# Optimization experiments

Hardware: AMD Instinct MI355X
Metric: run time of the kernel (lower is better)

The kernel has to match this reference:

```python
import jax, jax.numpy as jnp
import numpy as np

K = 3          # spatial kernel partitions
EPS = 1e-5     # BatchNorm eps


def setup_inputs() -> dict:
    key = jax.random.key(0)
    ks = jax.random.split(key, 5)
    N, C_in, T, V = 32, 64, 512, 27
    C_out = 128
    return {
        "x": jax.random.normal(ks[0], (N, C_in, T, V), dtype=jnp.float32),
        "len_x": 512,
        "conv_w": jax.random.normal(ks[1], (C_out * K, C_in, 1, 1), dtype=jnp.float32) * 0.05,
        "conv_b": jax.random.normal(ks[2], (C_out * K,), dtype=jnp.float32) * 0.05,
        "A": jax.random.uniform(ks[3], (K, V, V), dtype=jnp.float32),
        "gamma": jnp.ones((C_out,), dtype=jnp.float32),
        "beta": jnp.zeros((C_out,), dtype=jnp.float32),
    }


def reference(x, len_x, conv_w, conv_b, A, gamma, beta):
    # Pointwise conv (kernel (1,1)): [N,C_in,T,V] x [K*C_out,C_in] -> [N,K*C_out,T,V]
    w = conv_w[:, :, 0, 0]
    y = jnp.einsum('nctv,oc->notv', x, w) + conv_b[None, :, None, None]
    n, kc, t, v = y.shape
    y = y.reshape(n, K, kc // K, t, v)
    # Graph aggregation over adjacency partitions
    z = jnp.einsum('nkctv,kvw->nctw', y, A)
    # BatchNorm2d (training mode: batch stats, biased variance) + ReLU
    mean = jnp.mean(z, axis=(0, 2, 3), keepdims=True)
    var = jnp.mean((z - mean) ** 2, axis=(0, 2, 3), keepdims=True)
    zn = (z - mean) * jax.lax.rsqrt(var + EPS)
    out = zn * gamma[None, :, None, None] + beta[None, :, None, None]
    return jax.nn.relu(out)
```

## Files before the change

kernel.cpp:

```cpp
#include <hip/hip_runtime.h>
#include <cstdint>
#include <cstddef>

#define NT_TOTAL 16384
#define R_NT 8
#define NBLK 2048
#define CNT_F 442368.0f

#define XA_OFF 0
#define XA_STRIDE 400
#define R2_OFF 102400
#define XS_STRIDE 80
#define WBT_STRIDE 400
#define CB_OFF 153600
#define SA_OFF 155136
#define ST_OFF 155520
#define LDS_BYTES 156544
#define ZL_STRIDE 260

typedef __attribute__((ext_vector_type(8))) short short8;
typedef __attribute__((ext_vector_type(4))) float f32x4;

__device__ __forceinline__ unsigned short f2bf(float f) {
  unsigned int u = __float_as_uint(f);
  u = u + 0x7FFFu + ((u >> 16) & 1u);
  return (unsigned short)(u >> 16);
}
__device__ __forceinline__ float bf2f(unsigned short b) {
  return __uint_as_float(((unsigned int)b) << 16);
}

template <bool ZBF16>
__global__ __launch_bounds__(512, 2) void gcn_k1(
    const float* __restrict__ x, const float* __restrict__ cw,
    const float* __restrict__ cb, const float* __restrict__ A,
    float* __restrict__ zout_f32, unsigned short* __restrict__ zout_bf16,
    float* __restrict__ partial) {
  extern __shared__ char smem[];
  const int tid = threadIdx.x;
  const int lane = tid & 63;
  const int wid = tid >> 6;
  const int blk = blockIdx.x;
  const int nt0 = blk * R_NT;

  const int ci = tid & 63;
  const int r = wid;
  const int ntI = nt0 + r;
  const int nI = ntI >> 9;
  const int tI = ntI & 511;
  const float* xr = x + ((size_t)(nI * 64 + ci) * 512 + tI) * 27;
  float xrow[27];
#pragma unroll
  for (int v = 0; v < 27; ++v) xrow[v] = xr[v];

  float2 wreg[24];
  {
    const float2* cw2 = (const float2*)cw;
#pragma unroll
    for (int i = 0; i < 24; ++i) {
      const int p = i * 512 + tid;
      const int c = p / 96;
      const int kp = p % 96;
      const int k = kp >> 5;
      const int cip = kp & 31;
      wreg[i] = cw2[(k * 128 + c) * 32 + cip];
    }
  }

  short8 aop[3][2];
#pragma unroll
  for (int k = 0; k < 3; ++k)
#pragma unroll
    for (int mt = 0; mt < 2; ++mt) {
      const int wr = mt * 16 + (lane & 15);
#pragma unroll
      for (int j = 0; j < 8; ++j) {
        const int v = (lane >> 4) * 8 + j;
        float val = (wr < 27 && v < 27) ? A[k * 729 + v * 27 + wr] : 0.f;
        aop[k][mt][j] = (short)f2bf(val);
      }
    }

  if (tid < 256) ((float*)(smem + ST_OFF))[tid] = 0.f;
  if (tid < 384) ((float*)(smem + CB_OFF))[tid] = cb[tid];
  if (tid < 81) {
    const int k = tid / 27, w = tid % 27;
    float s = 0.f;
#pragma unroll
    for (int v = 0; v < 27; ++v) s += A[k * 729 + v * 27 + w];
    ((float*)(smem + SA_OFF))[k * 32 + w] = s;
  }
  {
    char* base = smem + R2_OFF + r * (64 * XS_STRIDE) + ci * XS_STRIDE;
#pragma unroll
    for (int i = 0; i < 16; ++i) {
      const int v0 = 2 * i, v1 = 2 * i + 1;
      unsigned int b0 = (v0 < 27) ? (unsigned int)f2bf(xrow[v0]) : 0u;
      unsigned int b1 = (v1 < 27) ? (unsigned int)f2bf(xrow[v1]) : 0u;
      *(unsigned int*)(base + i * 4) = b0 | (b1 << 16);
    }
  }
  __syncthreads();

  {
    const int r2 = wid;
    short8 bfr[4];
#pragma unroll
    for (int nt2 = 0; nt2 < 4; ++nt2) {
      const int ci2 = nt2 * 16 + (lane & 15);
      bfr[nt2] = *(const short8*)(smem + R2_OFF + r2 * (64 * XS_STRIDE) +
                                  ci2 * XS_STRIDE + (lane >> 4) * 16);
    }
#pragma unroll
    for (int k = 0; k < 3; ++k)
#pragma unroll
      for (int mt = 0; mt < 2; ++mt)
#pragma unroll
        for (int nt2 = 0; nt2 < 4; ++nt2) {
          f32x4 d = {0.f, 0.f, 0.f, 0.f};
          d = __builtin_amdgcn_mfma_f32_16x16x32_bf16(aop[k][mt], bfr[nt2], d, 0, 0, 0);
          const int ciW = nt2 * 16 + (lane & 15);
#pragma unroll
          for (int reg = 0; reg < 4; ++reg) {
            const int w = mt * 16 + (lane >> 4) * 4 + reg;
            if (w < 27) {
              const int m = r2 * 32 + w;
              *(unsigned short*)(smem + XA_OFF + m * XA_STRIDE + (k * 64 + ciW) * 2) =
                  f2bf(d[reg]);
            }
          }
        }
  }
  __syncthreads();

#pragma unroll
  for (int i = 0; i < 24; ++i) {
    const int p = i * 512 + tid;
    const int c = p / 96;
    const int kp = p % 96;
    unsigned int b0 = f2bf(wreg[i].x);
    unsigned int b1 = f2bf(wreg[i].y);
    *(unsigned int*)(smem + R2_OFF + c * WBT_STRIDE + kp * 4) = b0 | (b1 << 16);
  }
  __syncthreads();

  const int mgrp = wid >> 1;
  const int ngrp = wid & 1;
  f32x4 acc[4][4];
#pragma unroll
  for (int a = 0; a < 4; ++a)
#pragma unroll
    for (int b = 0; b < 4; ++b) acc[a][b] = (f32x4){0.f, 0.f, 0.f, 0.f};

#pragma unroll
  for (int ks = 0; ks < 6; ++ks) {
    short8 afr[4], bfr2[4];
#pragma unroll
    for (int mt = 0; mt < 4; ++mt) {
      const int m = mgrp * 64 + mt * 16 + (lane & 15);
      afr[mt] = *(const short8*)(smem + XA_OFF + m * XA_STRIDE + ks * 64 + (lane >> 4) * 16);
    }
#pragma unroll
    for (int ntt = 0; ntt < 4; ++ntt) {
      const int c = ngrp * 64 + ntt * 16 + (lane & 15);
      bfr2[ntt] = *(const short8*)(smem + R2_OFF + c * WBT_STRIDE + ks * 64 + (lane >> 4) * 16);
    }
#pragma unroll
    for (int mt = 0; mt < 4; ++mt)
#pragma unroll
      for (int ntt = 0; ntt < 4; ++ntt)
        acc[mt][ntt] =
            __builtin_amdgcn_mfma_f32_16x16x32_bf16(afr[mt], bfr2[ntt], acc[mt][ntt], 0, 0, 0);
  }
  __syncthreads();

  {
    const float* cbl = (const float*)(smem + CB_OFF);
    const float* sal = (const float*)(smem + SA_OFF);
    float* stats = (float*)(smem + ST_OFF);
    float cb0[4], cb1[4], cb2[4];
    int cc[4];
#pragma unroll
    for (int ntt = 0; ntt < 4; ++ntt) {
      cc[ntt] = ngrp * 64 + ntt * 16 + (lane & 15);
      cb0[ntt] = cbl[cc[ntt]];
      cb1[ntt] = cbl[128 + cc[ntt]];
      cb2[ntt] = cbl[256 + cc[ntt]];
    }
    float s1[4] = {0.f, 0.f, 0.f, 0.f}, s2[4] = {0.f, 0.f, 0.f, 0.f};
#pragma unroll
    for (int mt = 0; mt < 4; ++mt)
#pragma unroll
      for (int reg = 0; reg < 4; ++reg) {
        const int m = mgrp * 64 + mt * 16 + (lane >> 4) * 4 + reg;
        const int w = m & 31;
        if (w < 27) {
          const float sa0 = sal[w], sa1 = sal[32 + w], sa2 = sal[64 + w];
#pragma unroll
          for (int ntt = 0; ntt < 4; ++ntt) {
            float val = acc[mt][ntt][reg] + cb0[ntt] * sa0 + cb1[ntt] * sa1 + cb2[ntt] * sa2;
            s1[ntt] += val;
            s2[ntt] += val * val;
            *(unsigned short*)(smem + m * ZL_STRIDE + cc[ntt] * 2) = f2bf(val);
          }
        }
      }
#pragma unroll
    for (int ntt = 0; ntt < 4; ++ntt) {
      float a1 = s1[ntt], a2 = s2[ntt];
      a1 += __shfl_xor(a1, 16); a1 += __shfl_xor(a1, 32);
      a2 += __shfl_xor(a2, 16); a2 += __shfl_xor(a2, 32);
      if ((lane & 48) == 0) {
        atomicAdd(&stats[cc[ntt]], a1);
        atomicAdd(&stats[128 + cc[ntt]], a2);
      }
    }
  }
  __syncthreads();

  {
    const int n3 = nt0 >> 9;
    const int t0 = nt0 & 511;
    if (ZBF16) {
#pragma unroll 4
      for (int i = 0; i < 27; ++i) {
        const int idx = i * 512 + tid;
        const int c = idx / 108;
        const int jp = idx % 108;
        const int j0 = jp * 2, j1 = j0 + 1;
        const int tl0 = j0 / 27, w0 = j0 % 27;
        const int tl1 = j1 / 27, w1 = j1 % 27;
        unsigned int b0 = *(unsigned short*)(smem + (tl0 * 32 + w0) * ZL_STRIDE + c * 2);
        unsigned int b1 = *(unsigned short*)(smem + (tl1 * 32 + w1) * ZL_STRIDE + c * 2);
        const size_t base_e = ((size_t)(n3 * 128 + c) * 512 + t0) * 27;
        *(unsigned int*)((char*)zout_bf16 + base_e * 2 + (size_t)jp * 4) = b0 | (b1 << 16);
      }
    } else {
#pragma unroll 4
      for (int i = 0; i < 54; ++i) {
        const int idx = i * 512 + tid;
        const int c = idx / 216;
        const int j = idx % 216;
        const int tl = j / 27, w = j % 27;
        float v = bf2f(*(unsigned short*)(smem + (tl * 32 + w) * ZL_STRIDE + c * 2));
        zout_f32[((size_t)(n3 * 128 + c) * 512 + (t0 + tl)) * 27 + w] = v;
      }
    }
    if (tid < 256) partial[blk * 256 + tid] = ((float*)(smem + ST_OFF))[tid];
  }
}

__global__ __launch_bounds__(256) void gcn_k2(const float* __restrict__ partial,
                                              const float* __restrict__ gamma,
                                              const float* __restrict__ beta,
                                              float* __restrict__ ss) {
  __shared__ float lds[256];
  const int tid = threadIdx.x;
  float a0 = 0.f, a1 = 0.f, a2 = 0.f, a3 = 0.f;
  for (int b = 0; b < NBLK; b += 4) {
    a0 += partial[(b + 0) * 256 + tid];
    a1 += partial[(b + 1) * 256 + tid];
    a2 += partial[(b + 2) * 256 + tid];
    a3 += partial[(b + 3) * 256 + tid];
  }
  lds[tid] = (a0 + a1) + (a2 + a3);
  __syncthreads();
  if (tid < 128) {
    const float inv = 1.f / CNT_F;
    float mean = lds[tid] * inv;
    float var = lds[128 + tid] * inv - mean * mean;
    float rstd = rsqrtf(var + 1e-5f);
    float sc = gamma[tid] * rstd;
    ss[tid] = sc;
    ss[128 + tid] = beta[tid] - mean * sc;
  }
}

template <bool ZBF16>
__global__ __launch_bounds__(256) void gcn_k3(const unsigned short* __restrict__ zbf,
                                              float* __restrict__ out,
                                              const float* __restrict__ ss) {
  const int blk = blockIdx.x;
  const int tid = threadIdx.x;
  const int c = blk & 127;
  const float sc = ss[c];
  const float sh = ss[128 + c];
  float4* op = (float4*)out + (size_t)blk * 3456;
  if (ZBF16) {
    const ushort4* zp = (const ushort4*)zbf + (size_t)blk * 3456;
#pragma unroll 4
    for (int i = 0; i < 14; ++i) {
      const int idx = i * 256 + tid;
      if (idx < 3456) {
        ushort4 zv = zp[idx];
        float4 o;
        o.x = fmaxf(bf2f(zv.x) * sc + sh, 0.f);
        o.y = fmaxf(bf2f(zv.y) * sc + sh, 0.f);
        o.z = fmaxf(bf2f(zv.z) * sc + sh, 0.f);
        o.w = fmaxf(bf2f(zv.w) * sc + sh, 0.f);
        op[idx] = o;
      }
    }
  } else {
#pragma unroll 4
    for (int i = 0; i < 14; ++i) {
      const int idx = i * 256 + tid;
      if (idx < 3456) {
        float4 zv = op[idx];
        float4 o;
        o.x = fmaxf(zv.x * sc + sh, 0.f);
        o.y = fmaxf(zv.y * sc + sh, 0.f);
        o.z = fmaxf(zv.z * sc + sh, 0.f);
        o.w = fmaxf(zv.w * sc + sh, 0.f);
        op[idx] = o;
      }
    }
  }
}

extern "C" void kernel_launch(void* const* d_in, const int* in_sizes, int n_in,
                              void* d_out, int out_size, void* d_ws, size_t ws_size,
                              hipStream_t stream) {
  (void)in_sizes; (void)n_in; (void)out_size;
  const float* x = (const float*)d_in[0];
  const float* cw = (const float*)d_in[2];
  const float* cb = (const float*)d_in[3];
  const float* A = (const float*)d_in[4];
  const float* gm = (const float*)d_in[5];
  const float* bt = (const float*)d_in[6];
  float* out = (float*)d_out;

  const size_t Z_BYTES = (size_t)56623104 * 2;
  const size_t PART_F = (size_t)NBLK * 256;
  const bool zbf16 = ws_size >= Z_BYTES + PART_F * 4 + 1024;

  if (zbf16) {
    unsigned short* zws = (unsigned short*)d_ws;
    float* partial = (float*)((char*)d_ws + Z_BYTES);
    float* ss = partial + PART_F;
    hipFuncSetAttribute((const void*)gcn_k1<true>,
                        hipFuncAttributeMaxDynamicSharedMemorySize, LDS_BYTES);
    gcn_k1<true><<<NBLK, 512, LDS_BYTES, stream>>>(x, cw, cb, A, nullptr, zws, partial);
    gcn_k2<<<1, 256, 0, stream>>>(partial, gm, bt, ss);
    gcn_k3<true><<<4096, 256, 0, stream>>>(zws, out, ss);
  } else {
    float* partial = (float*)d_ws;
    float* ss = partial + PART_F;
    hipFuncSetAttribute((const void*)gcn_k1<false>,
                        hipFuncAttributeMaxDynamicSharedMemorySize, LDS_BYTES);
    gcn_k1<false><<<NBLK, 512, LDS_BYTES, stream>>>(x, cw, cb, A, out, nullptr, partial);
    gcn_k2<<<1, 256, 0, stream>>>(partial, gm, bt, ss);
    gcn_k3<false><<<4096, 256, 0, stream>>>(nullptr, out, ss);
  }
}
```

Before: 542.2 us.

## Precompute bf16 weights and bias, shrink tiles, raise occupancy, split stats reduction

```diff
diff --git a/kernel.cpp b/kernel.cpp
--- a/kernel.cpp
+++ b/kernel.cpp
@@ -2,21 +2,24 @@
 #include <cstdint>
 #include <cstddef>
 
-#define NT_TOTAL 16384
-#define R_NT 8
-#define NBLK 2048
+#define R_NT 4
+#define NBLK 4096
 #define CNT_F 442368.0f
 
-#define XA_OFF 0
 #define XA_STRIDE 400
-#define R2_OFF 102400
+#define XS_OFF 51200
 #define XS_STRIDE 80
-#define WBT_STRIDE 400
-#define CB_OFF 153600
-#define SA_OFF 155136
-#define ST_OFF 155520
-#define LDS_BYTES 156544
-#define ZL_STRIDE 260
+#define ST_OFF 71680
+#define LDS_BYTES 72704
+#define ZL_STRIDE 264
+
+#define Z_BYTES   113246208ull
+#define WBT_SZ    49152
+#define B2_SZ     16384
+#define AOP_SZ    6144
+#define SS_SZ     1024
+#define PART2_SZ  65536
+#define PART_SZ   4194304
 
 typedef __attribute__((ext_vector_type(8))) short short8;
 typedef __attribute__((ext_vector_type(4))) float f32x4;
@@ -30,10 +33,49 @@
   return __uint_as_float(((unsigned int)b) << 16);
 }
 
+__global__ __launch_bounds__(256) void gcn_k0(const float* __restrict__ cw,
+                                              const float* __restrict__ cb,
+                                              const float* __restrict__ A,
+                                              unsigned short* __restrict__ wbt,
+                                              float* __restrict__ bias2,
+                                              unsigned short* __restrict__ aopt) {
+  const int idx = blockIdx.x * 256 + threadIdx.x;
+  if (idx < 12288) {
+    const int c = idx / 96, p = idx - c * 96;
+    const int k = p >> 5, ci0 = (p & 31) * 2;
+    const float* src = cw + ((size_t)(k * 128 + c)) * 64 + ci0;
+    ((unsigned int*)wbt)[idx] = (unsigned int)f2bf(src[0]) | ((unsigned int)f2bf(src[1]) << 16);
+  } else if (idx < 16384) {
+    const int e = idx - 12288;
+    const int c = e >> 5, w = e & 31;
+    float val = 0.f;
+    if (w < 27) {
+#pragma unroll
+      for (int k = 0; k < 3; ++k) {
+        float sa = 0.f;
+#pragma unroll
+        for (int v = 0; v < 27; ++v) sa += A[k * 729 + v * 27 + w];
+        val += cb[k * 128 + c] * sa;
+      }
+    }
+    bias2[e] = val;
+  } else if (idx < 17920) {
+    const int e2 = (idx - 16384) * 2;
+    const int k = e2 >> 10, rem = e2 & 1023;
+    const int mt = rem >> 9, rem2 = rem & 511;
+    const int ln = rem2 >> 3, j0 = rem2 & 7;
+    const int wr = mt * 16 + (ln & 15);
+    const int v0 = (ln >> 4) * 8 + j0, v1 = v0 + 1;
+    float f0 = (wr < 27 && v0 < 27) ? A[k * 729 + v0 * 27 + wr] : 0.f;
+    float f1 = (wr < 27 && v1 < 27) ? A[k * 729 + v1 * 27 + wr] : 0.f;
+    ((unsigned int*)aopt)[idx - 16384] = (unsigned int)f2bf(f0) | ((unsigned int)f2bf(f1) << 16);
+  }
+}
+
 template <bool ZBF16>
-__global__ __launch_bounds__(512, 2) void gcn_k1(
-    const float* __restrict__ x, const float* __restrict__ cw,
-    const float* __restrict__ cb, const float* __restrict__ A,
+__global__ __launch_bounds__(512, 4) void gcn_k1(
+    const float* __restrict__ x, const unsigned short* __restrict__ wbt,
+    const float* __restrict__ bias2, const unsigned short* __restrict__ aopt,
     float* __restrict__ zout_f32, unsigned short* __restrict__ zout_bf16,
     float* __restrict__ partial) {
   extern __shared__ char smem[];
@@ -42,169 +84,130 @@
   const int wid = tid >> 6;
   const int blk = blockIdx.x;
   const int nt0 = blk * R_NT;
-
-  const int ci = tid & 63;
-  const int r = wid;
-  const int ntI = nt0 + r;
-  const int nI = ntI >> 9;
-  const int tI = ntI & 511;
-  const float* xr = x + ((size_t)(nI * 64 + ci) * 512 + tI) * 27;
-  float xrow[27];
-#pragma unroll
-  for (int v = 0; v < 27; ++v) xrow[v] = xr[v];
-
-  float2 wreg[24];
+  const int n = nt0 >> 9;
+  const int t0 = nt0 & 511;
+
+  short8 aop[3][2];
+#pragma unroll
+  for (int k = 0; k < 3; ++k)
+#pragma unroll
+    for (int mt = 0; mt < 2; ++mt)
+      aop[k][mt] = *(const short8*)(aopt + ((k * 2 + mt) * 64 + lane) * 8);
+
   {
-    const float2* cw2 = (const float2*)cw;
-#pragma unroll
-    for (int i = 0; i < 24; ++i) {
-      const int p = i * 512 + tid;
-      const int c = p / 96;
-      const int kp = p % 96;
-      const int k = kp >> 5;
-      const int cip = kp & 31;
-      wreg[i] = cw2[(k * 128 + c) * 32 + cip];
-    }
-  }
-
-  short8 aop[3][2];
-#pragma unroll
-  for (int k = 0; k < 3; ++k)
-#pragma unroll
-    for (int mt = 0; mt < 2; ++mt) {
-      const int wr = mt * 16 + (lane & 15);
-#pragma unroll
-      for (int j = 0; j < 8; ++j) {
-        const int v = (lane >> 4) * 8 + j;
-        float val = (wr < 27 && v < 27) ? A[k * 729 + v * 27 + wr] : 0.f;
-        aop[k][mt][j] = (short)f2bf(val);
-      }
-    }
-
+    const int idx = tid >> 1, h = tid & 1;
+    const int r = idx >> 6, ci = idx & 63;
+    const float* xr = x + ((size_t)(n * 64 + ci) * 512 + t0 + r) * 27;
+    unsigned int* row = (unsigned int*)(smem + XS_OFF + (r * 64 + ci) * XS_STRIDE);
+    if (h == 0) {
+      float f[14];
+#pragma unroll
+      for (int v = 0; v < 14; ++v) f[v] = xr[v];
+#pragma unroll
+      for (int p = 0; p < 7; ++p)
+        row[p] = (unsigned int)f2bf(f[2 * p]) | ((unsigned int)f2bf(f[2 * p + 1]) << 16);
+    } else {
+      float f[13];
+#pragma unroll
+      for (int v = 0; v < 13; ++v) f[v] = xr[14 + v];
+#pragma unroll
+      for (int p = 7; p < 16; ++p) {
+        const int v0 = 2 * p - 14, v1 = v0 + 1;
+        unsigned int b0 = (v0 < 13) ? (unsigned int)f2bf(f[v0]) : 0u;
+        unsigned int b1 = (v1 < 13) ? (unsigned int)f2bf(f[v1]) : 0u;
+        row[p] = b0 | (b1 << 16);
+      }
+    }
+  }
   if (tid < 256) ((float*)(smem + ST_OFF))[tid] = 0.f;
-  if (tid < 384) ((float*)(smem + CB_OFF))[tid] = cb[tid];
-  if (tid < 81) {
-    const int k = tid / 27, w = tid % 27;
-    float s = 0.f;
-#pragma unroll
-    for (int v = 0; v < 27; ++v) s += A[k * 729 + v * 27 + w];
-    ((float*)(smem + SA_OFF))[k * 32 + w] = s;
-  }
+  __syncthreads();
+
   {
-    char* base = smem + R2_OFF + r * (64 * XS_STRIDE) + ci * XS_STRIDE;
-#pragma unroll
-    for (int i = 0; i < 16; ++i) {
-      const int v0 = 2 * i, v1 = 2 * i + 1;
-      unsigned int b0 = (v0 < 27) ? (unsigned int)f2bf(xrow[v0]) : 0u;
-      unsigned int b1 = (v1 < 27) ? (unsigned int)f2bf(xrow[v1]) : 0u;
-      *(unsigned int*)(base + i * 4) = b0 | (b1 << 16);
-    }
-  }
-  __syncthreads();
-
-  {
-    const int r2 = wid;
-    short8 bfr[4];
-#pragma unroll
-    for (int nt2 = 0; nt2 < 4; ++nt2) {
-      const int ci2 = nt2 * 16 + (lane & 15);
-      bfr[nt2] = *(const short8*)(smem + R2_OFF + r2 * (64 * XS_STRIDE) +
-                                  ci2 * XS_STRIDE + (lane >> 4) * 16);
+    const int r2 = wid >> 1, half = wid & 1;
+    short8 bfr[2];
+#pragma unroll
+    for (int nt2 = 0; nt2 < 2; ++nt2) {
+      const int ci2 = half * 32 + nt2 * 16 + (lane & 15);
+      bfr[nt2] = *(const short8*)(smem + XS_OFF + (r2 * 64 + ci2) * XS_STRIDE + (lane >> 4) * 16);
     }
 #pragma unroll
     for (int k = 0; k < 3; ++k)
 #pragma unroll
       for (int mt = 0; mt < 2; ++mt)
 #pragma unroll
-        for (int nt2 = 0; nt2 < 4; ++nt2) {
+        for (int nt2 = 0; nt2 < 2; ++nt2) {
           f32x4 d = {0.f, 0.f, 0.f, 0.f};
           d = __builtin_amdgcn_mfma_f32_16x16x32_bf16(aop[k][mt], bfr[nt2], d, 0, 0, 0);
-          const int ciW = nt2 * 16 + (lane & 15);
+          const int ciW = half * 32 + nt2 * 16 + (lane & 15);
+          const int wb = mt * 16 + (lane >> 4) * 4;
 #pragma unroll
           for (int reg = 0; reg < 4; ++reg) {
-            const int w = mt * 16 + (lane >> 4) * 4 + reg;
-            if (w < 27) {
-              const int m = r2 * 32 + w;
-              *(unsigned short*)(smem + XA_OFF + m * XA_STRIDE + (k * 64 + ciW) * 2) =
-                  f2bf(d[reg]);
-            }
+            const int m = r2 * 32 + wb + reg;
+            *(unsigned short*)(smem + m * XA_STRIDE + (k * 64 + ciW) * 2) = f2bf(d[reg]);
           }
         }
   }
   __syncthreads();
 
-#pragma unroll
-  for (int i = 0; i < 24; ++i) {
-    const int p = i * 512 + tid;
-    const int c = p / 96;
-    const int kp = p % 96;
-    unsigned int b0 = f2bf(wreg[i].x);
-    unsigned int b1 = f2bf(wreg[i].y);
-    *(unsigned int*)(smem + R2_OFF + c * WBT_STRIDE + kp * 4) = b0 | (b1 << 16);
-  }
-  __syncthreads();
-
   const int mgrp = wid >> 1;
   const int ngrp = wid & 1;
-  f32x4 acc[4][4];
-#pragma unroll
-  for (int a = 0; a < 4; ++a)
+  f32x4 acc[2][4];
+#pragma unroll
+  for (int a = 0; a < 2; ++a)
 #pragma unroll
     for (int b = 0; b < 4; ++b) acc[a][b] = (f32x4){0.f, 0.f, 0.f, 0.f};
 
-#pragma unroll
+#pragma unroll 2
   for (int ks = 0; ks < 6; ++ks) {
-    short8 afr[4], bfr2[4];
-#pragma unroll
-    for (int mt = 0; mt < 4; ++mt) {
-      const int m = mgrp * 64 + mt * 16 + (lane & 15);
-      afr[mt] = *(const short8*)(smem + XA_OFF + m * XA_STRIDE + ks * 64 + (lane >> 4) * 16);
+    short8 afr[2], bfrg[4];
+#pragma unroll
+    for (int mt = 0; mt < 2; ++mt) {
+      const int m = mgrp * 32 + mt * 16 + (lane & 15);
+      afr[mt] = *(const short8*)(smem + m * XA_STRIDE + ks * 64 + (lane >> 4) * 16);
     }
 #pragma unroll
     for (int ntt = 0; ntt < 4; ++ntt) {
       const int c = ngrp * 64 + ntt * 16 + (lane & 15);
-      bfr2[ntt] = *(const short8*)(smem + R2_OFF + c * WBT_STRIDE + ks * 64 + (lane >> 4) * 16);
-    }
-#pragma unroll
-    for (int mt = 0; mt < 4; ++mt)
+      bfrg[ntt] = *(const short8*)(wbt + c * 192 + ks * 32 + (lane >> 4) * 8);
+    }
+#pragma unroll
+    for (int mt = 0; mt < 2; ++mt)
 #pragma unroll
       for (int ntt = 0; ntt < 4; ++ntt)
         acc[mt][ntt] =
-            __builtin_amdgcn_mfma_f32_16x16x32_bf16(afr[mt], bfr2[ntt], acc[mt][ntt], 0, 0, 0);
+            __builtin_amdgcn_mfma_f32_16x16x32_bf16(afr[mt], bfrg[ntt], acc[mt][ntt], 0, 0, 0);
   }
   __syncthreads();
 
   {
-    const float* cbl = (const float*)(smem + CB_OFF);
-    const float* sal = (const float*)(smem + SA_OFF);
     float* stats = (float*)(smem + ST_OFF);
-    float cb0[4], cb1[4], cb2[4];
     int cc[4];
 #pragma unroll
-    for (int ntt = 0; ntt < 4; ++ntt) {
-      cc[ntt] = ngrp * 64 + ntt * 16 + (lane & 15);
-      cb0[ntt] = cbl[cc[ntt]];
-      cb1[ntt] = cbl[128 + cc[ntt]];
-      cb2[ntt] = cbl[256 + cc[ntt]];
-    }
+    for (int ntt = 0; ntt < 4; ++ntt) cc[ntt] = ngrp * 64 + ntt * 16 + (lane & 15);
     float s1[4] = {0.f, 0.f, 0.f, 0.f}, s2[4] = {0.f, 0.f, 0.f, 0.f};
 #pragma unroll
-    for (int mt = 0; mt < 4; ++mt)
+    for (int mt = 0; mt < 2; ++mt) {
+      const int mb = mgrp * 32 + mt * 16 + (lane >> 4) * 4;
+      unsigned int pk[4][2];
+#pragma unroll
+      for (int ntt = 0; ntt < 4; ++ntt) { pk[ntt][0] = 0u; pk[ntt][1] = 0u; }
 #pragma unroll
       for (int reg = 0; reg < 4; ++reg) {
-        const int m = mgrp * 64 + mt * 16 + (lane >> 4) * 4 + reg;
-        const int w = m & 31;
+        const int w = (mb + reg) & 31;
         if (w < 27) {
-          const float sa0 = sal[w], sa1 = sal[32 + w], sa2 = sal[64 + w];
 #pragma unroll
           for (int ntt = 0; ntt < 4; ++ntt) {
-            float val = acc[mt][ntt][reg] + cb0[ntt] * sa0 + cb1[ntt] * sa1 + cb2[ntt] * sa2;
+            float val = acc[mt][ntt][reg] + bias2[cc[ntt] * 32 + w];
             s1[ntt] += val;
             s2[ntt] += val * val;
-            *(unsigned short*)(smem + m * ZL_STRIDE + cc[ntt] * 2) = f2bf(val);
+            pk[ntt][reg >> 1] |= ((unsigned int)f2bf(val)) << ((reg & 1) * 16);
           }
         }
       }
+#pragma unroll
+      for (int ntt = 0; ntt < 4; ++ntt)
+        *(uint2*)(smem + cc[ntt] * ZL_STRIDE + mb * 2) = make_uint2(pk[ntt][0], pk[ntt][1]);
+    }
 #pragma unroll
     for (int ntt = 0; ntt < 4; ++ntt) {
       float a1 = s1[ntt], a2 = s2[ntt];
@@ -218,52 +221,62 @@
   }
   __syncthreads();
 
-  {
-    const int n3 = nt0 >> 9;
-    const int t0 = nt0 & 511;
-    if (ZBF16) {
+  if (ZBF16) {
+#pragma unroll
+    for (int i = 0; i < 14; ++i) {
+      const int idx = i * 512 + tid;
+      if (idx < 6912) {
+        const int c = idx / 54;
+        const int d = idx - c * 54;
+        const int j0 = 2 * d, j1 = j0 + 1;
+        const int tl0 = j0 / 27, w0 = j0 - 27 * tl0;
+        const int tl1 = j1 / 27, w1 = j1 - 27 * tl1;
+        unsigned int b0 = *(unsigned short*)(smem + c * ZL_STRIDE + (tl0 * 32 + w0) * 2);
+        unsigned int b1 = *(unsigned short*)(smem + c * ZL_STRIDE + (tl1 * 32 + w1) * 2);
+        const size_t base = ((size_t)(n * 128 + c) * 512 + t0) * 27;
+        *(unsigned int*)((char*)zout_bf16 + base * 2 + (size_t)j0 * 2) = b0 | (b1 << 16);
+      }
+    }
+  } else {
+#pragma unroll
+    for (int i = 0; i < 27; ++i) {
+      const int idx = i * 512 + tid;
+      const int c = idx / 108;
+      const int d = idx - c * 108;
+      const int tl = d / 27, w = d - 27 * tl;
+      float v = bf2f(*(unsigned short*)(smem + c * ZL_STRIDE + (tl * 32 + w) * 2));
+      zout_f32[((size_t)(n * 128 + c) * 512 + (t0 + tl)) * 27 + w] = v;
+    }
+  }
+  if (tid < 256) partial[(size_t)blk * 256 + tid] = ((float*)(smem + ST_OFF))[tid];
+}
+
+__global__ __launch_bounds__(256) void gcn_k2a(const float* __restrict__ partial,
+                                               float* __restrict__ part2) {
+  const int b = blockIdx.x;
+  const int tid = threadIdx.x;
+  const float* p = partial + (size_t)b * 64 * 256 + tid;
+  float s0 = 0.f, s1 = 0.f, s2 = 0.f, s3 = 0.f;
 #pragma unroll 4
-      for (int i = 0; i < 27; ++i) {
-        const int idx = i * 512 + tid;
-        const int c = idx / 108;
-        const int jp = idx % 108;
-        const int j0 = jp * 2, j1 = j0 + 1;
-        const int tl0 = j0 / 27, w0 = j0 % 27;
-        const int tl1 = j1 / 27, w1 = j1 % 27;
-        unsigned int b0 = *(unsigned short*)(smem + (tl0 * 32 + w0) * ZL_STRIDE + c * 2);
-        unsigned int b1 = *(unsigned short*)(smem + (tl1 * 32 + w1) * ZL_STRIDE + c * 2);
-        const size_t base_e = ((size_t)(n3 * 128 + c) * 512 + t0) * 27;
-        *(unsigned int*)((char*)zout_bf16 + base_e * 2 + (size_t)jp * 4) = b0 | (b1 << 16);
-      }
-    } else {
-#pragma unroll 4
-      for (int i = 0; i < 54; ++i) {
-        const int idx = i * 512 + tid;
-        const int c = idx / 216;
-        const int j = idx % 216;
-        const int tl = j / 27, w = j % 27;
-        float v = bf2f(*(unsigned short*)(smem + (tl * 32 + w) * ZL_STRIDE + c * 2));
-        zout_f32[((size_t)(n3 * 128 + c) * 512 + (t0 + tl)) * 27 + w] = v;
-      }
-    }
-    if (tid < 256) partial[blk * 256 + tid] = ((float*)(smem + ST_OFF))[tid];
-  }
-}
-
-__global__ __launch_bounds__(256) void gcn_k2(const float* __restrict__ partial,
-                                              const float* __restrict__ gamma,
-                                              const float* __restrict__ beta,
-                                              float* __restrict__ ss) {
+  for (int r = 0; r < 64; r += 4) {
+    s0 += p[(r + 0) * 256];
+    s1 += p[(r + 1) * 256];
+    s2 += p[(r + 2) * 256];
+    s3 += p[(r + 3) * 256];
+  }
+  part2[b * 256 + tid] = (s0 + s1) + (s2 + s3);
+}
+
+__global__ __launch_bounds__(256) void gcn_k2b(const float* __restrict__ part2,
+                                               const float* __restrict__ gamma,
+                                               const float* __restrict__ beta,
+                                               float* __restrict__ ss) {
   __shared__ float lds[256];
   const int tid = threadIdx.x;
-  float a0 = 0.f, a1 = 0.f, a2 = 0.f, a3 = 0.f;
-  for (int b = 0; b < NBLK; b += 4) {
-    a0 += partial[(b + 0) * 256 + tid];
-    a1 += partial[(b + 1) * 256 + tid];
-    a2 += partial[(b + 2) * 256 + tid];
-    a3 += partial[(b + 3) * 256 + tid];
-  }
-  lds[tid] = (a0 + a1) + (a2 + a3);
+  float s = 0.f;
+#pragma unroll 4
+  for (int r = 0; r < 64; ++r) s += part2[r * 256 + tid];
+  lds[tid] = s;
   __syncthreads();
   if (tid < 128) {
     const float inv = 1.f / CNT_F;
@@ -330,26 +343,34 @@
   const float* bt = (const float*)d_in[6];
   float* out = (float*)d_out;
 
-  const size_t Z_BYTES = (size_t)56623104 * 2;
-  const size_t PART_F = (size_t)NBLK * 256;
-  const bool zbf16 = ws_size >= Z_BYTES + PART_F * 4 + 1024;
+  const size_t need_bf16 = Z_BYTES + WBT_SZ + B2_SZ + AOP_SZ + SS_SZ + PART2_SZ + PART_SZ;
+  const bool zbf16 = ws_size >= need_bf16;
+  const size_t zoff = zbf16 ? Z_BYTES : 0;
+
+  char* base = (char*)d_ws;
+  unsigned short* wbt = (unsigned short*)(base + zoff);
+  float* bias2 = (float*)(base + zoff + WBT_SZ);
+  unsigned short* aopt = (unsigned short*)(base + zoff + WBT_SZ + B2_SZ);
+  float* ssv = (float*)(base + zoff + WBT_SZ + B2_SZ + AOP_SZ);
+  float* part2 = (float*)(base + zoff + WBT_SZ + B2_SZ + AOP_SZ + SS_SZ);
+  float* partial = (float*)(base + zoff + WBT_SZ + B2_SZ + AOP_SZ + SS_SZ + PART2_SZ);
+
+  gcn_k0<<<70, 256, 0, stream>>>(cw, cb, A, wbt, bias2, aopt);
 
   if (zbf16) {
     unsigned short* zws = (unsigned short*)d_ws;
-    float* partial = (float*)((char*)d_ws + Z_BYTES);
-    float* ss = partial + PART_F;
     hipFuncSetAttribute((const void*)gcn_k1<true>,
                         hipFuncAttributeMaxDynamicSharedMemorySize, LDS_BYTES);
-    gcn_k1<true><<<NBLK, 512, LDS_BYTES, stream>>>(x, cw, cb, A, nullptr, zws, partial);
-    gcn_k2<<<1, 256, 0, stream>>>(partial, gm, bt, ss);
-    gcn_k3<true><<<4096, 256, 0, stream>>>(zws, out, ss);
+    gcn_k1<true><<<NBLK, 512, LDS_BYTES, stream>>>(x, wbt, bias2, aopt, nullptr, zws, partial);
+    gcn_k2a<<<64, 256, 0, stream>>>(partial, part2);
+    gcn_k2b<<<1, 256, 0, stream>>>(part2, gm, bt, ssv);
+    gcn_k3<true><<<4096, 256, 0, stream>>>(zws, out, ssv);
   } else {
-    float* partial = (float*)d_ws;
-    float* ss = partial + PART_F;
     hipFuncSetAttribute((const void*)gcn_k1<false>,
                         hipFuncAttributeMaxDynamicSharedMemorySize, LDS_BYTES);
-    gcn_k1<false><<<NBLK, 512, LDS_BYTES, stream>>>(x, cw, cb, A, out, nullptr, partial);
-    gcn_k2<<<1, 256, 0, stream>>>(partial, gm, bt, ss);
-    gcn_k3<false><<<4096, 256, 0, stream>>>(nullptr, out, ss);
-  }
-}
+    gcn_k1<false><<<NBLK, 512, LDS_BYTES, stream>>>(x, wbt, bias2, aopt, out, nullptr, partial);
+    gcn_k2a<<<64, 256, 0, stream>>>(partial, part2);
+    gcn_k2b<<<1, 256, 0, stream>>>(part2, gm, bt, ssv);
+    gcn_k3<false><<<4096, 256, 0, stream>>>(nullptr, out, ssv);
+  }
+}
```

New measurement: 537.3 us. No clear change (-0.9%).
